# Performance work log

Hardware: AMD Instinct MI355X
Metric: run time of the kernel (lower is better)

## Reference

```python
import math
import jax, jax.numpy as jnp
import numpy as np

D_MODEL = 1024
NHEAD = 16
NUM_TEMP = 4
HEAD = D_MODEL // NHEAD          # 64
DIM = HEAD // NUM_TEMP           # 16
SCALE = math.sqrt(HEAD)
B, L = 2, 2048


def _make_freq():
    # freq = 10000^(-arange(0,dim,2)/dim), repeat_interleave(2) -> length DIM
    f = np.power(10000.0, -np.arange(0, DIM, 2) / DIM)
    return jnp.asarray(np.repeat(f, 2), dtype=jnp.float32)  # (DIM,)


def setup_inputs() -> dict:
    key = jax.random.key(0)
    ks = jax.random.split(key, 8)
    s = 0.02
    return {
        "data": jax.random.normal(ks[0], (B, L, D_MODEL), jnp.float32),
        "temporal": jax.random.uniform(ks[1], (B, L, NUM_TEMP), jnp.float32),
        "mask": jnp.zeros((L, L), jnp.float32),
        "Wq": jax.random.normal(ks[2], (D_MODEL, D_MODEL), jnp.float32) * s,
        "bq": jnp.zeros((D_MODEL,), jnp.float32),
        "Wk": jax.random.normal(ks[3], (D_MODEL, D_MODEL), jnp.float32) * s,
        "bk": jnp.zeros((D_MODEL,), jnp.float32),
        "Wv": jax.random.normal(ks[4], (D_MODEL, D_MODEL), jnp.float32) * s,
        "bv": jnp.zeros((D_MODEL,), jnp.float32),
    }


def _rotate_half_pairs(x):
    # [-x2, x1, -x4, x3, ...] along last dim
    stacked = jnp.stack([-x[..., 1::2], x[..., 0::2]], axis=-1)
    return stacked.reshape(x.shape)


def _apply_rotary(x, sine, cosine):
    # x: (B,L,H,HEAD); sine/cosine: (B,L,HEAD)
    return x * cosine[:, :, None, :] + _rotate_half_pairs(x) * sine[:, :, None, :]


def reference(data, temporal, mask, Wq, bq, Wk, bk, Wv, bv):
    freq = _make_freq()  # (DIM,)
    b, l, _ = data.shape
    q = (data @ Wq + bq).reshape(b, l, NHEAD, HEAD)
    k = (data @ Wk + bk).reshape(b, l, NHEAD, HEAD)
    v = (data @ Wv + bv).reshape(b, l, NHEAD, HEAD)
    # per-temporal-column frequencies: (B,L,T,DIM) -> (B,L,HEAD)
    freqs = (temporal[..., None] * freq).reshape(b, l, HEAD)
    cosine = jnp.cos(freqs)
    sine = jnp.sin(freqs)
    rq = _apply_rotary(q, sine, cosine)
    rk = _apply_rotary(k, sine, cosine)
    logits = jnp.einsum("bqhs,bkhs->bhqk", rq, rk) / SCALE + mask
    weights = jax.nn.softmax(logits, axis=-1)  # dropout is identity at eval
    context = jnp.einsum("bhqk,bkhs->bqhs", weights, v)
    return context.reshape(b, l, D_MODEL)
```

## Files before the change

### kernel.cpp

```cpp
#include <hip/hip_runtime.h>
#include <hip/hip_bf16.h>

#define LSEQ 2048
#define DM   1024
#define NH   16

typedef __attribute__((ext_vector_type(8)))  short bf16x8;
typedef __attribute__((ext_vector_type(8)))  unsigned short u16x8;
typedef __attribute__((ext_vector_type(4)))  float f32x4;
typedef __attribute__((ext_vector_type(16))) float f32x16;
typedef __attribute__((ext_vector_type(4)))  unsigned int u32x4;

#define LOG2E 1.4426950408889634f
#define C1SC  0.18033688011112042f
#define DEFER_THR 8.0f

static __device__ __forceinline__ float exp2fast(float x) {
  return __builtin_amdgcn_exp2f(x);
}

static __device__ __forceinline__ unsigned short f2bf(float f) {
  unsigned int u = __float_as_uint(f);
  u += 0x7FFFu + ((u >> 16) & 1u);
  return (unsigned short)(u >> 16);
}

static __device__ __forceinline__ unsigned pk2(float a, float b) {
  __hip_bfloat162 t = __float22bfloat162_rn(make_float2(a, b));
  return *reinterpret_cast<unsigned*>(&t);
}

static __device__ __forceinline__ f32x16 unpack16(u16x8 a, u16x8 b) {
  const u32x4 ua = __builtin_bit_cast(u32x4, a);
  const u32x4 ub = __builtin_bit_cast(u32x4, b);
  f32x16 r;
#pragma unroll
  for (int i = 0; i < 4; ++i) {
    r[2 * i]     = __uint_as_float(ua[i] << 16);
    r[2 * i + 1] = __uint_as_float(ua[i] & 0xFFFF0000u);
    r[8 + 2 * i]     = __uint_as_float(ub[i] << 16);
    r[8 + 2 * i + 1] = __uint_as_float(ub[i] & 0xFFFF0000u);
  }
  return r;
}

static __device__ __forceinline__ bf16x8 mkfrag(int hi, float p0, float p1,
                                                float p2, float p3, float p4,
                                                float p5, float p6, float p7) {
  unsigned w0 = pk2(p0, p1), w1 = pk2(p2, p3);
  unsigned w2 = pk2(p4, p5), w3 = pk2(p6, p7);
  unsigned s0 = hi ? w0 : w2, s1 = hi ? w1 : w3;
  unsigned t0 = __shfl_xor(s0, 32, 64);
  unsigned t1 = __shfl_xor(s1, 32, 64);
  u32x4 f;
  f[0] = hi ? t0 : w0;
  f[1] = hi ? t1 : w1;
  f[2] = hi ? w2 : t0;
  f[3] = hi ? w3 : t1;
  return __builtin_bit_cast(bf16x8, f);
}

static __device__ __forceinline__ void gld_lds16(const unsigned short* g, unsigned short* l) {
  __builtin_amdgcn_global_load_lds(
      (const __attribute__((address_space(1))) unsigned int*)g,
      (__attribute__((address_space(3))) unsigned int*)l, 16, 0, 0);
}

__global__ void k_convert_data(const float* __restrict__ src,
                               unsigned short* __restrict__ dst, int n4) {
  int i = blockIdx.x * 256 + threadIdx.x;
  if (i >= n4) return;
  float4 v = reinterpret_cast<const float4*>(src)[i];
  ushort4 o;
  o.x = f2bf(v.x); o.y = f2bf(v.y); o.z = f2bf(v.z); o.w = f2bf(v.w);
  reinterpret_cast<ushort4*>(dst)[i] = o;
}

__global__ void k_transpose_w(const float* __restrict__ Wq,
                              const float* __restrict__ Wk,
                              const float* __restrict__ Wv,
                              unsigned short* __restrict__ Wt) {
  __shared__ unsigned short tile[64][65];
  const float* W = (blockIdx.z == 0) ? Wq : (blockIdx.z == 1) ? Wk : Wv;
  int n0 = blockIdx.x * 64, k0 = blockIdx.y * 64;
  int t = threadIdx.x;
  int c = t & 63, r0 = t >> 6;
  for (int i = 0; i < 16; ++i) {
    int r = r0 + i * 4;
    tile[r][c] = f2bf(W[(size_t)(k0 + r) * DM + n0 + c]);
  }
  __syncthreads();
  size_t nbase = (size_t)blockIdx.z * DM + n0;
  for (int i = 0; i < 16; ++i) {
    int n = r0 + i * 4;
    Wt[(nbase + n) * DM + k0 + c] = tile[c][n];
  }
}

__global__ void k_maskC(const float* __restrict__ mask,
                        unsigned short* __restrict__ maskCb) {
  __shared__ float tile[64][65];
  int q0 = blockIdx.x * 64, kv0 = blockIdx.y * 64;
  int t = threadIdx.x;
  int c = t & 63, r0 = t >> 6;
  for (int i = 0; i < 16; ++i) {
    int r = r0 + i * 4;
    tile[r][c] = mask[(size_t)(q0 + r) * LSEQ + kv0 + c];
  }
  __syncthreads();
  const int q = t & 63, slot = t >> 6;
  const int tt = slot >> 1, hh = slot & 1;
  u16x8 va, vb;
#pragma unroll
  for (int r = 0; r < 8; ++r) {
    const int kvloc = 32 * tt + 4 * hh + (r & 3) + 8 * (r >> 2);
    va[r] = f2bf(tile[q][kvloc] * LOG2E);
  }
#pragma unroll
  for (int r = 8; r < 16; ++r) {
    const int kvloc = 32 * tt + 4 * hh + (r & 3) + 8 * (r >> 2);
    vb[r - 8] = f2bf(tile[q][kvloc] * LOG2E);
  }
  unsigned short* dst = maskCb + ((size_t)((kv0 >> 6) * 4 + slot) * 2048 + q0 + q) * 16;
  *reinterpret_cast<u16x8*>(dst) = va;
  *reinterpret_cast<u16x8*>(dst + 8) = vb;
}

__global__ __launch_bounds__(256) void k_qkv_gemm(
    const unsigned short* __restrict__ A, const unsigned short* __restrict__ Bt,
    const float* __restrict__ bq, const float* __restrict__ bk,
    const float* __restrict__ bv, const float* __restrict__ temporal,
    unsigned short* __restrict__ qbuf, unsigned short* __restrict__ kbuf,
    unsigned short* __restrict__ vtbuf) {
  __shared__ unsigned short As[128 * 32];
  __shared__ unsigned short Bs[128 * 32];
  __shared__ unsigned short otile[128 * 136];
  const int tid = threadIdx.x;
  const int lane = tid & 63, wid = tid >> 6;
  const int wm = wid >> 1, wn = wid & 1;
  const int lr = lane & 15, lg = lane >> 4;

  const int bid = blockIdx.x;
  const int xcd = bid & 7, rr = bid >> 3;
  const int mblk = xcd * 4 + (rr / 24);
  const int nblk = rr % 24;
  const int m0 = mblk * 128;
  const int n0 = nblk * 128;

  f32x4 acc[4][4] = {};

  const int e0 = tid * 8;
  const int e1 = (256 + tid) * 8;
  const int ra0 = e0 >> 5, ca0 = e0 & 31;
  const int ra1 = e1 >> 5, ca1 = e1 & 31;
  unsigned short* lA0 = As + wid * 512;
  unsigned short* lA1 = As + 2048 + wid * 512;
  unsigned short* lB0 = Bs + wid * 512;
  unsigned short* lB1 = Bs + 2048 + wid * 512;

  for (int k0 = 0; k0 < DM; k0 += 32) {
    __syncthreads();
    gld_lds16(A + (size_t)(m0 + ra0) * DM + k0 + ca0, lA0);
    gld_lds16(A + (size_t)(m0 + ra1) * DM + k0 + ca1, lA1);
    gld_lds16(Bt + (size_t)(n0 + ra0) * DM + k0 + ca0, lB0);
    gld_lds16(Bt + (size_t)(n0 + ra1) * DM + k0 + ca1, lB1);
    __syncthreads();
    bf16x8 af[4], bfv[4];
    for (int mi = 0; mi < 4; ++mi)
      af[mi] = *reinterpret_cast<const bf16x8*>(As + (wm * 64 + mi * 16 + lr) * 32 + lg * 8);
    for (int ni = 0; ni < 4; ++ni)
      bfv[ni] = *reinterpret_cast<const bf16x8*>(Bs + (wn * 64 + ni * 16 + lr) * 32 + lg * 8);
    for (int mi = 0; mi < 4; ++mi)
      for (int ni = 0; ni < 4; ++ni)
        acc[mi][ni] = __builtin_amdgcn_mfma_f32_16x16x32_bf16(af[mi], bfv[ni], acc[mi][ni], 0, 0, 0);
  }

  const int mat = n0 >> 10;
  const int c0 = n0 & 1023;
  const int bb = m0 >> 11;
  const int mloc = m0 & 2047;
  const float qscale = (mat == 0) ? C1SC : 1.f;

  for (int mi = 0; mi < 4; ++mi) {
    const int rrel_base = wm * 64 + mi * 16 + lg * 4;
    for (int ni = 0; ni < 4; ++ni) {
      const int crel = wn * 64 + ni * 16 + lr;
      const int c = (c0 + crel);
      const int d = c & 63;
      const float bias = (mat == 0 ? bq : mat == 1 ? bk : bv)[c];
      f32x4 v = acc[mi][ni];
      if (mat < 2) {
        const int jj = d & 15, tt = d >> 4;
        const float fr = __expf(-(float)(jj & 14) * 0.5756462732485115f);
        const float sign = (d & 1) ? 1.f : -1.f;
        for (int j = 0; j < 4; ++j) {
          const int rrel = rrel_base + j;
          const float x = v[j] + bias;
          const float part = __shfl_xor(x, 1, 64);
          const int lqs = mloc + rrel;
          const float fq = temporal[((size_t)bb * LSEQ + lqs) * 4 + tt] * fr;
          float sn, cs;
          __sincosf(fq, &sn, &cs);
          otile[rrel * 136 + crel] = f2bf((x * cs + sign * part * sn) * qscale);
        }
      } else {
        for (int j = 0; j < 4; ++j) {
          const int rrel = rrel_base + j;
          otile[crel * 136 + rrel] = f2bf(v[j] + bias);
        }
      }
    }
  }
  __syncthreads();

  for (int i = 0; i < 2; ++i) {
    const int h = (c0 >> 6) + i;
    const size_t bh = (size_t)(bb * NH + h);
    if (mat == 0) {
      const size_t base = (bh * LSEQ + mloc) * 64;
#pragma unroll
      for (int kk2 = 0; kk2 < 4; ++kk2) {
        const int e = kk2 * 2048 + tid * 8;
        const int r = e >> 6, d = e & 63;
        *reinterpret_cast<u16x8*>(qbuf + base + e) =
            *reinterpret_cast<const u16x8*>(otile + r * 136 + i * 64 + d);
      }
    } else if (mat == 1) {
      const size_t base = bh * 131072 + (size_t)(mloc >> 5) * 2048;
#pragma unroll
      for (int kk2 = 0; kk2 < 4; ++kk2) {
        const int e = kk2 * 2048 + tid * 8;
        const int r = kk2 * 32 + ((tid >> 1) & 31);
        const int d = ((tid >> 6) & 3) * 16 + (tid & 1) * 8;
        *reinterpret_cast<u16x8*>(kbuf + base + e) =
            *reinterpret_cast<const u16x8*>(otile + r * 136 + i * 64 + d);
      }
    } else {
      const size_t base = bh * 131072 + (size_t)(mloc >> 4) * 1024;
#pragma unroll
      for (int kk2 = 0; kk2 < 4; ++kk2) {
        const int e = kk2 * 2048 + tid * 8;
        const int d = ((tid >> 6) & 1) * 32 + ((tid >> 1) & 31);
        const int r = (kk2 * 2 + (tid >> 7)) * 16 + (tid & 1) * 8;
        *reinterpret_cast<u16x8*>(vtbuf + base + e) =
            *reinterpret_cast<const u16x8*>(otile + (i * 64 + d) * 136 + r);
      }
    }
  }
}

__global__ __launch_bounds__(256) void k_attn(
    const unsigned short* __restrict__ qbuf, const unsigned short* __restrict__ kbuf,
    const unsigned short* __restrict__ vtbuf, const unsigned short* __restrict__ maskCb,
    float* __restrict__ out) {
  __shared__ float otile[4][64][33];
  const int tid = threadIdx.x, lane = tid & 63, wid = tid >> 6;
  const int lq = lane & 31, hi = lane >> 5;
  const int bh = blockIdx.y;
  const int q0 = blockIdx.x * 128 + wid * 32;
  const int qg = q0 + lq;
  const size_t bhL = (size_t)bh * LSEQ;
  const unsigned short* kb = kbuf + (size_t)bh * 131072;
  const unsigned short* vb = vtbuf + (size_t)bh * 131072;
  const unsigned short* mb = maskCb + ((size_t)hi * 2048 + qg) * 16;

  bf16x8 qf[4];
#pragma unroll
  for (int c = 0; c < 4; ++c)
    qf[c] = *reinterpret_cast<const bf16x8*>(qbuf + (bhL + qg) * 64 + c * 16 + hi * 8);

  f32x16 o0 = {}, o1 = {};
  float m2 = -1e30f, l_run = 0.f;

  for (int kv0 = 0; kv0 < LSEQ; kv0 += 64) {
    const unsigned short* mt = mb + (size_t)(kv0 >> 6) * (4 * 2048 * 16);
    f32x16 s0 = unpack16(*reinterpret_cast<const u16x8*>(mt),
                         *reinterpret_cast<const u16x8*>(mt + 8));
    f32x16 s1 = unpack16(*reinterpret_cast<const u16x8*>(mt + 2 * 2048 * 16),
                         *reinterpret_cast<const u16x8*>(mt + 2 * 2048 * 16 + 8));

    const unsigned short* kch = kb + (size_t)(kv0 >> 5) * 2048;
#pragma unroll
    for (int c = 0; c < 4; ++c) {
      bf16x8 k0 = *reinterpret_cast<const bf16x8*>(kch + c * 512 + lq * 16 + hi * 8);
      bf16x8 k1 = *reinterpret_cast<const bf16x8*>(kch + 2048 + c * 512 + lq * 16 + hi * 8);
      s0 = __builtin_amdgcn_mfma_f32_32x32x16_bf16(k0, qf[c], s0, 0, 0, 0);
      s1 = __builtin_amdgcn_mfma_f32_32x32x16_bf16(k1, qf[c], s1, 0, 0, 0);
    }

    float t0[8];
#pragma unroll
    for (int r = 0; r < 8; ++r) t0[r] = fmaxf(fmaxf(s0[r], s0[r + 8]), fmaxf(s1[r], s1[r + 8]));
#pragma unroll
    for (int r = 0; r < 4; ++r) t0[r] = fmaxf(t0[r], t0[r + 4]);
    float loc = fmaxf(fmaxf(t0[0], t0[1]), fmaxf(t0[2], t0[3]));
    loc = fmaxf(loc, __shfl_xor(loc, 32, 64));

    if (!__all(loc <= m2 + DEFER_THR)) {
      const float mn = fmaxf(m2, loc);
      const float al = exp2fast(m2 - mn);
      l_run *= al;
#pragma unroll
      for (int r = 0; r < 16; ++r) { o0[r] *= al; o1[r] *= al; }
      m2 = mn;
    }

    float rs0 = 0.f, rs1 = 0.f, rs2 = 0.f, rs3 = 0.f;
#pragma unroll
    for (int r = 0; r < 4; ++r) {
      s0[r] = exp2fast(s0[r] - m2);      rs0 += s0[r];
      s0[r + 4] = exp2fast(s0[r + 4] - m2);  rs1 += s0[r + 4];
      s0[r + 8] = exp2fast(s0[r + 8] - m2);  rs2 += s0[r + 8];
      s0[r + 12] = exp2fast(s0[r + 12] - m2); rs3 += s0[r + 12];
    }
#pragma unroll
    for (int r = 0; r < 4; ++r) {
      s1[r] = exp2fast(s1[r] - m2);      rs0 += s1[r];
      s1[r + 4] = exp2fast(s1[r + 4] - m2);  rs1 += s1[r + 4];
      s1[r + 8] = exp2fast(s1[r + 8] - m2);  rs2 += s1[r + 8];
      s1[r + 12] = exp2fast(s1[r + 12] - m2); rs3 += s1[r + 12];
    }
    float rs = (rs0 + rs1) + (rs2 + rs3);
    rs += __shfl_xor(rs, 32, 64);
    l_run += rs;

    bf16x8 pf0 = mkfrag(hi, s0[0], s0[1], s0[2], s0[3], s0[4], s0[5], s0[6], s0[7]);
    bf16x8 pf1 = mkfrag(hi, s0[8], s0[9], s0[10], s0[11], s0[12], s0[13], s0[14], s0[15]);
    bf16x8 pf2 = mkfrag(hi, s1[0], s1[1], s1[2], s1[3], s1[4], s1[5], s1[6], s1[7]);
    bf16x8 pf3 = mkfrag(hi, s1[8], s1[9], s1[10], s1[11], s1[12], s1[13], s1[14], s1[15]);

    const unsigned short* vch = vb + (size_t)(kv0 >> 4) * 1024;
#pragma unroll
    for (int ks = 0; ks < 4; ++ks) {
      bf16x8 pf = (ks == 0) ? pf0 : (ks == 1) ? pf1 : (ks == 2) ? pf2 : pf3;
      bf16x8 v0 = *reinterpret_cast<const bf16x8*>(vch + ks * 1024 + lq * 16 + hi * 8);
      bf16x8 v1 = *reinterpret_cast<const bf16x8*>(vch + ks * 1024 + 512 + lq * 16 + hi * 8);
      o0 = __builtin_amdgcn_mfma_f32_32x32x16_bf16(v0, pf, o0, 0, 0, 0);
      o1 = __builtin_amdgcn_mfma_f32_32x32x16_bf16(v1, pf, o1, 0, 0, 0);
    }
  }

  const float inv = 1.f / l_run;
#pragma unroll
  for (int r = 0; r < 16; ++r) {
    const int d = (r & 3) + 8 * (r >> 2) + 4 * hi;
    otile[wid][d][lq] = o0[r] * inv;
    otile[wid][32 + d][lq] = o1[r] * inv;
  }
  __syncthreads();
  const int b = bh >> 4, h = bh & 15;
#pragma unroll
  for (int i = 0; i < 8; ++i) {
    const int u = i * 64 + lane;
    const int q = u >> 4, c4 = u & 15;
    float4 w;
    w.x = otile[wid][c4 * 4 + 0][q];
    w.y = otile[wid][c4 * 4 + 1][q];
    w.z = otile[wid][c4 * 4 + 2][q];
    w.w = otile[wid][c4 * 4 + 3][q];
    *reinterpret_cast<float4*>(out + ((size_t)(b * LSEQ + q0 + q)) * DM + h * 64 + c4 * 4) = w;
  }
}

extern "C" void kernel_launch(void* const* d_in, const int* in_sizes, int n_in,
                              void* d_out, int out_size, void* d_ws, size_t ws_size,
                              hipStream_t stream) {
  const float* data     = (const float*)d_in[0];
  const float* temporal = (const float*)d_in[1];
  const float* mask     = (const float*)d_in[2];
  const float* Wq       = (const float*)d_in[3];
  const float* bq       = (const float*)d_in[4];
  const float* Wk       = (const float*)d_in[5];
  const float* bk       = (const float*)d_in[6];
  const float* Wv       = (const float*)d_in[7];
  const float* bv       = (const float*)d_in[8];
  float* out = (float*)d_out;

  char* ws = (char*)d_ws;
  unsigned short* data_bf = (unsigned short*)(ws);
  unsigned short* wt      = (unsigned short*)(ws + (size_t)8  * 1048576);
  unsigned short* qbuf    = (unsigned short*)(ws + (size_t)14 * 1048576);
  unsigned short* kbuf    = (unsigned short*)(ws + (size_t)22 * 1048576);
  unsigned short* vtbuf   = (unsigned short*)(ws + (size_t)30 * 1048576);
  unsigned short* maskCb  = data_bf;

  hipLaunchKernelGGL(k_convert_data, dim3(4096), dim3(256), 0, stream,
                     data, data_bf, (2 * LSEQ * DM) / 4);
  hipLaunchKernelGGL(k_transpose_w, dim3(16, 16, 3), dim3(256), 0, stream,
                     Wq, Wk, Wv, wt);
  hipLaunchKernelGGL(k_qkv_gemm, dim3(768), dim3(256), 0, stream,
                     data_bf, wt, bq, bk, bv, temporal, qbuf, kbuf, vtbuf);
  hipLaunchKernelGGL(k_maskC, dim3(32, 32), dim3(256), 0, stream,
                     mask, maskCb);
  hipLaunchKernelGGL(k_attn, dim3(16, 32), dim3(256), 0, stream,
                     qbuf, kbuf, vtbuf, maskCb, out);
}
```

Baseline: 138.4 us.

## Split KV range across wave pairs in attention and merge partial softmax states

Each attention block now covers 64 queries instead of 128. Its four waves form two query groups times two halves of the KV range, and each wave runs its online softmax over 1024 keys. The partial max and sum are exchanged through shared memory and combined with rescaling, and the two partial outputs are added before the global store. The grid doubles to 1024 blocks to raise occupancy and parallelism on the MI355X's many CUs. The cost is one extra sync and shared-memory reduction per block, plus twice the per-block Q and mask loads relative to the keys processed.

```diff
diff --git a/kernel.cpp b/kernel.cpp
--- a/kernel.cpp
+++ b/kernel.cpp
@@ -254,10 +254,12 @@
     const unsigned short* __restrict__ vtbuf, const unsigned short* __restrict__ maskCb,
     float* __restrict__ out) {
   __shared__ float otile[4][64][33];
+  __shared__ float mlbuf[4][32][2];
   const int tid = threadIdx.x, lane = tid & 63, wid = tid >> 6;
   const int lq = lane & 31, hi = lane >> 5;
+  const int qsub = wid & 1, kvh = wid >> 1;
   const int bh = blockIdx.y;
-  const int q0 = blockIdx.x * 128 + wid * 32;
+  const int q0 = blockIdx.x * 64 + qsub * 32;
   const int qg = q0 + lq;
   const size_t bhL = (size_t)bh * LSEQ;
   const unsigned short* kb = kbuf + (size_t)bh * 131072;
@@ -272,7 +274,8 @@
   f32x16 o0 = {}, o1 = {};
   float m2 = -1e30f, l_run = 0.f;
 
-  for (int kv0 = 0; kv0 < LSEQ; kv0 += 64) {
+  const int kv_beg = kvh * 1024, kv_end = kv_beg + 1024;
+  for (int kv0 = kv_beg; kv0 < kv_end; kv0 += 64) {
     const unsigned short* mt = mb + (size_t)(kv0 >> 6) * (4 * 2048 * 16);
     f32x16 s0 = unpack16(*reinterpret_cast<const u16x8*>(mt),
                          *reinterpret_cast<const u16x8*>(mt + 8));
@@ -340,25 +343,37 @@
     }
   }
 
-  const float inv = 1.f / l_run;
+  if (lane < 32) { mlbuf[wid][lq][0] = m2; mlbuf[wid][lq][1] = l_run; }
+  __syncthreads();
+  const int pw = wid ^ 2;
+  const float m_p = mlbuf[pw][lq][0];
+  const float l_p = mlbuf[pw][lq][1];
+  const float mstar = fmaxf(m2, m_p);
+  const float f  = exp2fast(m2 - mstar);
+  const float fp = exp2fast(m_p - mstar);
+  const float scale = f / (l_run * f + l_p * fp);
+
 #pragma unroll
   for (int r = 0; r < 16; ++r) {
     const int d = (r & 3) + 8 * (r >> 2) + 4 * hi;
-    otile[wid][d][lq] = o0[r] * inv;
-    otile[wid][32 + d][lq] = o1[r] * inv;
+    otile[wid][d][lq] = o0[r] * scale;
+    otile[wid][32 + d][lq] = o1[r] * scale;
   }
   __syncthreads();
+
   const int b = bh >> 4, h = bh & 15;
 #pragma unroll
-  for (int i = 0; i < 8; ++i) {
-    const int u = i * 64 + lane;
+  for (int i = 0; i < 4; ++i) {
+    const int u = i * 256 + tid;
     const int q = u >> 4, c4 = u & 15;
+    const int qs = q >> 5, ql = q & 31;
     float4 w;
-    w.x = otile[wid][c4 * 4 + 0][q];
-    w.y = otile[wid][c4 * 4 + 1][q];
-    w.z = otile[wid][c4 * 4 + 2][q];
-    w.w = otile[wid][c4 * 4 + 3][q];
-    *reinterpret_cast<float4*>(out + ((size_t)(b * LSEQ + q0 + q)) * DM + h * 64 + c4 * 4) = w;
+    w.x = otile[qs][c4 * 4 + 0][ql] + otile[2 + qs][c4 * 4 + 0][ql];
+    w.y = otile[qs][c4 * 4 + 1][ql] + otile[2 + qs][c4 * 4 + 1][ql];
+    w.z = otile[qs][c4 * 4 + 2][ql] + otile[2 + qs][c4 * 4 + 2][ql];
+    w.w = otile[qs][c4 * 4 + 3][ql] + otile[2 + qs][c4 * 4 + 3][ql];
+    *reinterpret_cast<float4*>(
+        out + ((size_t)(b * LSEQ + blockIdx.x * 64 + q)) * DM + h * 64 + c4 * 4) = w;
   }
 }
 
@@ -392,6 +407,6 @@
                      data_bf, wt, bq, bk, bv, temporal, qbuf, kbuf, vtbuf);
   hipLaunchKernelGGL(k_maskC, dim3(32, 32), dim3(256), 0, stream,
                      mask, maskCb);
-  hipLaunchKernelGGL(k_attn, dim3(16, 32), dim3(256), 0, stream,
+  hipLaunchKernelGGL(k_attn, dim3(32, 32), dim3(256), 0, stream,
                      qbuf, kbuf, vtbuf, maskCb, out);
 }
```

After: 140.3 us. Within noise of the previous version (+1.4%).
